# Performance work log

Measured on AMD Instinct MI355X. Metric: run time of the kernel, lower is better.

## Reference

```python
import jax, jax.numpy as jnp
import numpy as np

B, IN, OUT = 8192, 1024, 1024
GRID_SIZE, SPLINE_ORDER = 5, 3
GRID_LO, GRID_HI = -1.0, 1.0
LN_EPS = 1e-5


def make_grid():
    h = (GRID_HI - GRID_LO) / GRID_SIZE
    g = jnp.linspace(GRID_LO - h * SPLINE_ORDER, GRID_HI + h * SPLINE_ORDER,
                     GRID_SIZE + 2 * SPLINE_ORDER + 1, dtype=jnp.float32)
    return jnp.broadcast_to(g, (IN, g.shape[0]))  # [IN, 12]


def setup_inputs() -> dict:
    key = jax.random.key(0)
    k1, k2, k3 = jax.random.split(key, 3)
    # kaiming_uniform_ linear: bound = sqrt(3/fan_in)
    bw_bound = float(np.sqrt(3.0 / IN))
    sw_bound = float(np.sqrt(3.0 / (IN * 8)))
    return {
        "x": jax.random.normal(k1, (B, IN), dtype=jnp.float32),
        "base_weight": jax.random.uniform(k2, (OUT, IN), minval=-bw_bound, maxval=bw_bound, dtype=jnp.float32),
        "spline_weight": jax.random.uniform(k3, (OUT, IN, GRID_SIZE + SPLINE_ORDER), minval=-sw_bound, maxval=sw_bound, dtype=jnp.float32),
        "grid": make_grid(),
        "ln_gamma": jnp.ones((OUT,), dtype=jnp.float32),
        "ln_beta": jnp.zeros((OUT,), dtype=jnp.float32),
        "prelu_a": jnp.full((1,), 0.25, dtype=jnp.float32),
    }


def _bspline_bases(x, grid):
    # x: [B, IN]; grid: [IN, 12] -> bases: [B, IN, GRID_SIZE+SPLINE_ORDER]
    xu = x[:, :, None]                      # [B, IN, 1]
    g = grid[None, :, :]                    # [1, IN, 12]
    bases = ((xu >= g[..., :-1]) & (xu < g[..., 1:])).astype(x.dtype)
    for k in range(1, SPLINE_ORDER + 1):
        left = g[..., :-(k + 1)]
        right = g[..., k:-1]
        g_rshift = g[..., k + 1:]
        g_lshift = g[..., 1:-k]
        dr = right - left
        dd = g_rshift - g_lshift
        dr = jnp.where(dr == 0, jnp.ones_like(dr), dr)
        dd = jnp.where(dd == 0, jnp.ones_like(dd), dd)
        bases = (xu - left) / dr * bases[..., :-1] + (g_rshift - xu) / dd * bases[..., 1:]
    return bases


def reference(x, base_weight, spline_weight, grid, ln_gamma, ln_beta, prelu_a):
    base_out = jnp.dot(jax.nn.gelu(x, approximate=False), base_weight.T)  # [B, OUT]
    bases = _bspline_bases(x, grid)                                        # [B, IN, 8]
    spline_out = jnp.einsum('bik,oik->bo', bases, spline_weight)           # [B, OUT]
    y = base_out + spline_out
    mu = jnp.mean(y, axis=-1, keepdims=True)
    var = jnp.mean(jnp.square(y - mu), axis=-1, keepdims=True)
    yn = (y - mu) * jax.lax.rsqrt(var + LN_EPS) * ln_gamma + ln_beta
    return jnp.where(yn >= 0, yn, prelu_a * yn)
```

## Files before the change

### kernel.cpp

```cpp
#include <hip/hip_runtime.h>
#include <hip/hip_bf16.h>

typedef __attribute__((ext_vector_type(8))) short bf16x8;
typedef __attribute__((ext_vector_type(4))) float f32x4;

#define KTOT 9216
#define KHALF 4608
#define NB   8192
#define NIN  1024
#define NOUT 1024

__device__ __forceinline__ void load_lds16(const void* g, void* l) {
  __builtin_amdgcn_global_load_lds(
      (const __attribute__((address_space(1))) void*)g,
      (__attribute__((address_space(3))) void*)l, 16, 0, 0);
}

__global__ void prep(const float* __restrict__ x,
                     const float* __restrict__ grid,
                     __hip_bfloat16* __restrict__ A,
                     const float* __restrict__ bw,
                     const float* __restrict__ sw,
                     __hip_bfloat16* __restrict__ W) {
  if (blockIdx.x < 4096) {
    const int tid = blockIdx.x * blockDim.x + threadIdx.x;
    const int i  = tid & (NIN - 1);
    const int b0 = (tid >> 10) << 3;

    float g[12];
#pragma unroll
    for (int j = 0; j < 12; ++j) g[j] = grid[j];

    float invdr1[10], invdd1[10], invdr2[9], invdd2[9], invdr3[8], invdd3[8];
#pragma unroll
    for (int j = 0; j < 10; ++j) {
      invdr1[j] = __builtin_amdgcn_rcpf(g[j + 1] - g[j]);
      invdd1[j] = __builtin_amdgcn_rcpf(g[j + 2] - g[j + 1]);
    }
#pragma unroll
    for (int j = 0; j < 9; ++j) {
      invdr2[j] = __builtin_amdgcn_rcpf(g[j + 2] - g[j]);
      invdd2[j] = __builtin_amdgcn_rcpf(g[j + 3] - g[j + 1]);
    }
#pragma unroll
    for (int j = 0; j < 8; ++j) {
      invdr3[j] = __builtin_amdgcn_rcpf(g[j + 3] - g[j]);
      invdd3[j] = __builtin_amdgcn_rcpf(g[j + 4] - g[j + 1]);
    }

    for (int bb = 0; bb < 8; ++bb) {
      const int b = b0 + bb;
      const float xv = x[(size_t)b * NIN + i];
      const float ge = 0.5f * xv * (1.0f + erff(xv * 0.70710678118654752f));
      __hip_bfloat16* Arow = A + (size_t)b * KTOT;
      Arow[i] = __float2bfloat16(ge);

      float bas[11];
#pragma unroll
      for (int j = 0; j < 11; ++j)
        bas[j] = (xv >= g[j] && xv < g[j + 1]) ? 1.0f : 0.0f;
#pragma unroll
      for (int j = 0; j < 10; ++j)
        bas[j] = (xv - g[j]) * invdr1[j] * bas[j] + (g[j + 2] - xv) * invdd1[j] * bas[j + 1];
#pragma unroll
      for (int j = 0; j < 9; ++j)
        bas[j] = (xv - g[j]) * invdr2[j] * bas[j] + (g[j + 3] - xv) * invdd2[j] * bas[j + 1];
#pragma unroll
      for (int j = 0; j < 8; ++j)
        bas[j] = (xv - g[j]) * invdr3[j] * bas[j] + (g[j + 4] - xv) * invdd3[j] * bas[j + 1];

      union { __hip_bfloat16 h[8]; uint4 v; } u;
#pragma unroll
      for (int k = 0; k < 8; ++k) u.h[k] = __float2bfloat16(bas[k]);
      *reinterpret_cast<uint4*>(Arow + NIN + i * 8) = u.v;
    }
  } else {
    const int idx = (blockIdx.x - 4096) * blockDim.x + threadIdx.x;
    const int o  = idx / 1152;
    const int c8 = (idx - o * 1152) * 8;
    const float* src = (c8 < 1024) ? (bw + (size_t)o * 1024 + c8)
                                   : (sw + (size_t)o * 8192 + (c8 - 1024));
    float4 f0 = reinterpret_cast<const float4*>(src)[0];
    float4 f1 = reinterpret_cast<const float4*>(src)[1];
    union { __hip_bfloat16 h[8]; uint4 v; } u;
    u.h[0] = __float2bfloat16(f0.x); u.h[1] = __float2bfloat16(f0.y);
    u.h[2] = __float2bfloat16(f0.z); u.h[3] = __float2bfloat16(f0.w);
    u.h[4] = __float2bfloat16(f1.x); u.h[5] = __float2bfloat16(f1.y);
    u.h[6] = __float2bfloat16(f1.z); u.h[7] = __float2bfloat16(f1.w);
    *reinterpret_cast<uint4*>(W + (size_t)o * KTOT + c8) = u.v;
  }
}

__global__ __launch_bounds__(512, 2)
void gemm_8ph(const __hip_bfloat16* __restrict__ A,
              const __hip_bfloat16* __restrict__ Bw,
              float* __restrict__ P0,
              float* __restrict__ P1w) {
  extern __shared__ char smem[];

  const int tid  = threadIdx.x;
  const int lane = tid & 63;
  const int wave = tid >> 6;
  const int wr = wave >> 2;
  const int wc = wave & 3;

  const int orig = blockIdx.x;
  const int bid  = (orig & 7) * 32 + (orig >> 3);
  const int ks    = bid & 1;
  const int tileN = (bid >> 1) & 3;
  const int tileM = bid >> 3;
  const size_t brow = (size_t)tileM * 256;
  const size_t bcol = (size_t)tileN * 256;
  const int kbeg = ks * KHALF;

  const __hip_bfloat16* Ab = A  + brow * KTOT;
  const __hip_bfloat16* Bb = Bw + bcol * KTOT;
  float* C = ks ? P1w : P0;

  const int swsrc = ((tid & 7) ^ ((tid >> 3) & 7)) * 8;
  const __hip_bfloat16* srcA = Ab + (size_t)(tid >> 3) * KTOT + kbeg + swsrc;
  const __hip_bfloat16* srcB = Bb + (size_t)(tid >> 3) * KTOT + kbeg + swsrc;
  const int wdst = wave * 1024;

#define AHALF(buf, h) (smem + (buf) * 32768 + (h) * 16384)
#define BHALF(slot, h) (smem + 65536 + (slot) * 32768 + (h) * 16384)

  auto stageA = [&](int bufA, int h, int kt) {
    const __hip_bfloat16* g = srcA + (size_t)h * (128 * KTOT) + (size_t)kt * 64;
    char* d = AHALF(bufA, h) + wdst;
    load_lds16(g, d);
    load_lds16(g + (size_t)64 * KTOT, d + 8192);
  };
  auto stageB = [&](int slot, int h, int kt) {
    const __hip_bfloat16* g = srcB + (size_t)h * (128 * KTOT) + (size_t)kt * 64;
    char* d = BHALF(slot, h) + wdst;
    load_lds16(g, d);
    load_lds16(g + (size_t)64 * KTOT, d + 8192);
  };

  const int fr = lane & 15;
  const int hi = lane >> 4;
  const int sw = (fr & 7) << 4;
  const int ax0 = (hi * 16) ^ sw;
  const int ax1 = (64 + hi * 16) ^ sw;

  bf16x8 a[4][2], b[4][2];
  f32x4 acc[8][4] = {};

#define RD_A(CBA, MH) { \
    const char* Ah = AHALF(CBA, wr) + (MH) * 8192; \
    _Pragma("unroll") \
    for (int mi2 = 0; mi2 < 4; ++mi2) { \
      const char* p = Ah + (mi2 * 16 + fr) * 128; \
      a[mi2][0] = *(const bf16x8*)(p + ax0); \
      a[mi2][1] = *(const bf16x8*)(p + ax1); } }

#define RD_B(SB, NH) { \
    const char* Bh = BHALF(SB, wc >> 1) + ((wc & 1) * 64 + (NH) * 32) * 128; \
    _Pragma("unroll") \
    for (int ni2 = 0; ni2 < 2; ++ni2) { \
      const char* p = Bh + (ni2 * 16 + fr) * 128; \
      b[(NH) * 2 + ni2][0] = *(const bf16x8*)(p + ax0); \
      b[(NH) * 2 + ni2][1] = *(const bf16x8*)(p + ax1); } }

#define PH_SYNC() do { \
    asm volatile("" ::: "memory"); \
    __builtin_amdgcn_s_barrier(); \
    asm volatile("s_waitcnt lgkmcnt(0)" ::: "memory"); \
    __builtin_amdgcn_sched_barrier(0); } while (0)

#define QMFMA(MH, NH) do { \
    __builtin_amdgcn_s_setprio(1); \
    _Pragma("unroll") \
    for (int mi2 = 0; mi2 < 4; ++mi2) \
      _Pragma("unroll") \
      for (int ni2 = 0; ni2 < 2; ++ni2) \
        _Pragma("unroll") \
        for (int kk = 0; kk < 2; ++kk) \
          acc[(MH) * 4 + mi2][(NH) * 2 + ni2] = \
            __builtin_amdgcn_mfma_f32_16x16x32_bf16(a[mi2][kk], b[(NH) * 2 + ni2][kk], \
                                                    acc[(MH) * 4 + mi2][(NH) * 2 + ni2], 0, 0, 0); \
    __builtin_amdgcn_s_setprio(0); } while (0)

#define TILE(T, CBA, SB, SB2, STA, STB, VM2, VM4) do { \
     \
    RD_A(CBA, 0); RD_B(SB, 0); \
    if (STA) stageA((CBA) ^ 1, 0, (T) + 1); \
    PH_SYNC(); QMFMA(0, 0); \
     \
    RD_B(SB, 1); \
    if (STA) stageA((CBA) ^ 1, 1, (T) + 1); \
    asm volatile(VM2 ::: "memory"); \
    PH_SYNC(); QMFMA(0, 1); \
     \
    RD_A(CBA, 1); \
    if (STB) stageB(SB2, 0, (T) + 2); \
    PH_SYNC(); QMFMA(1, 1); \
     \
    if (STB) stageB(SB2, 1, (T) + 2); \
    asm volatile(VM4 ::: "memory"); \
    PH_SYNC(); QMFMA(1, 0); \
  } while (0)

  stageB(0, 0, 0); stageB(0, 1, 0);
  stageA(0, 0, 0); stageA(0, 1, 0);
  stageB(1, 0, 1); stageB(1, 1, 1);
  asm volatile("s_waitcnt vmcnt(6)" ::: "memory");
  __builtin_amdgcn_s_barrier();
  asm volatile("" ::: "memory");

  for (int it = 0; it < 11; ++it) {
    TILE(it * 6 + 0, 0, 0, 2, 1, 1, "s_waitcnt vmcnt(8)", "s_waitcnt vmcnt(6)");
    TILE(it * 6 + 1, 1, 1, 0, 1, 1, "s_waitcnt vmcnt(8)", "s_waitcnt vmcnt(6)");
    TILE(it * 6 + 2, 0, 2, 1, 1, 1, "s_waitcnt vmcnt(8)", "s_waitcnt vmcnt(6)");
    TILE(it * 6 + 3, 1, 0, 2, 1, 1, "s_waitcnt vmcnt(8)", "s_waitcnt vmcnt(6)");
    TILE(it * 6 + 4, 0, 1, 0, 1, 1, "s_waitcnt vmcnt(8)", "s_waitcnt vmcnt(6)");
    TILE(it * 6 + 5, 1, 2, 1, 1, 1, "s_waitcnt vmcnt(8)", "s_waitcnt vmcnt(6)");
  }
  TILE(66, 0, 0, 2, 1, 1, "s_waitcnt vmcnt(8)", "s_waitcnt vmcnt(6)");
  TILE(67, 1, 1, 0, 1, 1, "s_waitcnt vmcnt(8)", "s_waitcnt vmcnt(6)");
  TILE(68, 0, 2, 1, 1, 1, "s_waitcnt vmcnt(8)", "s_waitcnt vmcnt(6)");
  TILE(69, 1, 0, 2, 1, 1, "s_waitcnt vmcnt(8)", "s_waitcnt vmcnt(6)");
  TILE(70, 0, 1, 0, 1, 0, "s_waitcnt vmcnt(8)", "s_waitcnt vmcnt(2)");
  TILE(71, 1, 2, 1, 0, 0, "s_waitcnt vmcnt(0)", "s_nop 0");

#undef TILE
#undef QMFMA
#undef PH_SYNC
#undef RD_B
#undef RD_A
#undef BHALF
#undef AHALF

  const int crow0 = (lane >> 4) * 4;
#pragma unroll
  for (int mi = 0; mi < 8; ++mi)
#pragma unroll
    for (int ni = 0; ni < 4; ++ni) {
      const size_t r0 = brow + wr * 128 + mi * 16 + crow0;
      const size_t cc = bcol + wc * 64 + ni * 16 + fr;
      float* cp = C + r0 * NOUT + cc;
#pragma unroll
      for (int r = 0; r < 4; ++r) cp[(size_t)r * NOUT] = acc[mi][ni][r];
    }
}

__global__ void reduce_ln_prelu(const float* __restrict__ P0,
                                float* __restrict__ y,
                                const float* __restrict__ gamma,
                                const float* __restrict__ beta,
                                const float* __restrict__ pa) {
  const int row = blockIdx.x;
  const int t = threadIdx.x;
  const float* p0r = P0 + (size_t)row * NOUT;
  float* yr = y + (size_t)row * NOUT;

  float4 aa = reinterpret_cast<const float4*>(p0r)[t];
  float4 v = reinterpret_cast<const float4*>(yr)[t];
  v.x += aa.x; v.y += aa.y; v.z += aa.z; v.w += aa.w;

  float s  = v.x + v.y + v.z + v.w;
  float sq = v.x * v.x + v.y * v.y + v.z * v.z + v.w * v.w;
#pragma unroll
  for (int off = 32; off > 0; off >>= 1) {
    s  += __shfl_down(s, off);
    sq += __shfl_down(sq, off);
  }
  __shared__ float red[8];
  const int wv = t >> 6, lane = t & 63;
  if (lane == 0) { red[wv] = s; red[4 + wv] = sq; }
  __syncthreads();
  if (t == 0) {
    const float S = red[0] + red[1] + red[2] + red[3];
    const float Q = red[4] + red[5] + red[6] + red[7];
    const float mu = S * (1.0f / NOUT);
    const float var = Q * (1.0f / NOUT) - mu * mu;
    red[0] = mu;
    red[1] = rsqrtf(var + 1e-5f);
  }
  __syncthreads();
  const float mu = red[0], rs = red[1];
  const float aP = pa[0];
  const float4 g4 = reinterpret_cast<const float4*>(gamma)[t];
  const float4 b4 = reinterpret_cast<const float4*>(beta)[t];
  float o0 = (v.x - mu) * rs * g4.x + b4.x;
  float o1 = (v.y - mu) * rs * g4.y + b4.y;
  float o2 = (v.z - mu) * rs * g4.z + b4.z;
  float o3 = (v.w - mu) * rs * g4.w + b4.w;
  v.x = o0 >= 0.0f ? o0 : aP * o0;
  v.y = o1 >= 0.0f ? o1 : aP * o1;
  v.z = o2 >= 0.0f ? o2 : aP * o2;
  v.w = o3 >= 0.0f ? o3 : aP * o3;
  reinterpret_cast<float4*>(yr)[t] = v;
}

extern "C" void kernel_launch(void* const* d_in, const int* in_sizes, int n_in,
                              void* d_out, int out_size, void* d_ws, size_t ws_size,
                              hipStream_t stream) {
  const float* x     = (const float*)d_in[0];
  const float* bw    = (const float*)d_in[1];
  const float* sw    = (const float*)d_in[2];
  const float* grid  = (const float*)d_in[3];
  const float* gamma = (const float*)d_in[4];
  const float* beta  = (const float*)d_in[5];
  const float* pa    = (const float*)d_in[6];
  float* out = (float*)d_out;

  __hip_bfloat16* Abuf = (__hip_bfloat16*)d_ws;
  __hip_bfloat16* Wbuf = Abuf + (size_t)NB * KTOT;
  float* P0 = (float*)(Wbuf + (size_t)NOUT * KTOT);

  hipFuncSetAttribute(reinterpret_cast<const void*>(gemm_8ph),
                      hipFuncAttributeMaxDynamicSharedMemorySize, 163840);

  prep<<<4096 + 4608, 256, 0, stream>>>(x, grid, Abuf, bw, sw, Wbuf);
  gemm_8ph<<<(NB / 256) * (NOUT / 256) * 2, 512, 163840, stream>>>(Abuf, Wbuf, P0, out);
  reduce_ln_prelu<<<NB, 256, 0, stream>>>(P0, out, gamma, beta, pa);
}
```

Measured before the change: 198.7 us.

## Restructure GEMM pipeline to two phases per tile with triple-buffered A

Reworks the main GEMM k-loop from four barrier phases per K-tile to two. A is now triple-buffered (prefetched two tiles ahead) and B double-buffered (one tile ahead), where before A was double- and B triple-buffered. Each phase issues larger batches of LDS reads and MFMAs between barriers, cutting synchronisation overhead. In exchange there is less fine-grained interleaving of loads with compute, and B loads have less time to land, which could expose memory latency.

```diff
diff --git a/kernel.cpp b/kernel.cpp
--- a/kernel.cpp
+++ b/kernel.cpp
@@ -92,10 +92,10 @@
 }
 
 __global__ __launch_bounds__(512, 2)
-void gemm_8ph(const __hip_bfloat16* __restrict__ A,
-              const __hip_bfloat16* __restrict__ Bw,
-              float* __restrict__ P0,
-              float* __restrict__ P1w) {
+void gemm_2b(const __hip_bfloat16* __restrict__ A,
+             const __hip_bfloat16* __restrict__ Bw,
+             float* __restrict__ P0,
+             float* __restrict__ P1w) {
   extern __shared__ char smem[];
 
   const int tid  = threadIdx.x;
@@ -122,18 +122,18 @@
   const __hip_bfloat16* srcB = Bb + (size_t)(tid >> 3) * KTOT + kbeg + swsrc;
   const int wdst = wave * 1024;
 
-#define AHALF(buf, h) (smem + (buf) * 32768 + (h) * 16384)
-#define BHALF(slot, h) (smem + 65536 + (slot) * 32768 + (h) * 16384)
-
-  auto stageA = [&](int bufA, int h, int kt) {
+#define AB_(buf)  (smem + (buf) * 32768)
+#define BB_(slot) (smem + 98304 + (slot) * 32768)
+
+  auto stageA = [&](int buf, int h, int kt) {
     const __hip_bfloat16* g = srcA + (size_t)h * (128 * KTOT) + (size_t)kt * 64;
-    char* d = AHALF(bufA, h) + wdst;
+    char* d = AB_(buf) + h * 16384 + wdst;
     load_lds16(g, d);
     load_lds16(g + (size_t)64 * KTOT, d + 8192);
   };
   auto stageB = [&](int slot, int h, int kt) {
     const __hip_bfloat16* g = srcB + (size_t)h * (128 * KTOT) + (size_t)kt * 64;
-    char* d = BHALF(slot, h) + wdst;
+    char* d = BB_(slot) + h * 16384 + wdst;
     load_lds16(g, d);
     load_lds16(g + (size_t)64 * KTOT, d + 8192);
   };
@@ -147,16 +147,16 @@
   bf16x8 a[4][2], b[4][2];
   f32x4 acc[8][4] = {};
 
-#define RD_A(CBA, MH) { \
-    const char* Ah = AHALF(CBA, wr) + (MH) * 8192; \
+#define RD_A(BUF, MH) { \
+    const char* Ah = AB_(BUF) + wr * 16384 + (MH) * 8192; \
     _Pragma("unroll") \
     for (int mi2 = 0; mi2 < 4; ++mi2) { \
       const char* p = Ah + (mi2 * 16 + fr) * 128; \
       a[mi2][0] = *(const bf16x8*)(p + ax0); \
       a[mi2][1] = *(const bf16x8*)(p + ax1); } }
 
-#define RD_B(SB, NH) { \
-    const char* Bh = BHALF(SB, wc >> 1) + ((wc & 1) * 64 + (NH) * 32) * 128; \
+#define RD_B(SLOT, NH) { \
+    const char* Bh = BB_(SLOT) + (wc >> 1) * 16384 + ((wc & 1) * 64 + (NH) * 32) * 128; \
     _Pragma("unroll") \
     for (int ni2 = 0; ni2 < 2; ++ni2) { \
       const char* p = Bh + (ni2 * 16 + fr) * 128; \
@@ -182,55 +182,50 @@
                                                     acc[(MH) * 4 + mi2][(NH) * 2 + ni2], 0, 0, 0); \
     __builtin_amdgcn_s_setprio(0); } while (0)
 
-#define TILE(T, CBA, SB, SB2, STA, STB, VM2, VM4) do { \
+#define TILE(T, ABUF, A2, BSL, STB, STA, VMB) do { \
      \
-    RD_A(CBA, 0); RD_B(SB, 0); \
-    if (STA) stageA((CBA) ^ 1, 0, (T) + 1); \
-    PH_SYNC(); QMFMA(0, 0); \
+    RD_A(ABUF, 0); RD_B(BSL, 0); RD_B(BSL, 1); \
+    if (STB) { stageB((BSL) ^ 1, 0, (T) + 1); stageB((BSL) ^ 1, 1, (T) + 1); } \
+    PH_SYNC(); \
+    QMFMA(0, 0); QMFMA(0, 1); \
      \
-    RD_B(SB, 1); \
-    if (STA) stageA((CBA) ^ 1, 1, (T) + 1); \
-    asm volatile(VM2 ::: "memory"); \
-    PH_SYNC(); QMFMA(0, 1); \
-     \
-    RD_A(CBA, 1); \
-    if (STB) stageB(SB2, 0, (T) + 2); \
-    PH_SYNC(); QMFMA(1, 1); \
-     \
-    if (STB) stageB(SB2, 1, (T) + 2); \
-    asm volatile(VM4 ::: "memory"); \
-    PH_SYNC(); QMFMA(1, 0); \
+    RD_A(ABUF, 1); \
+    if (STA) { stageA(A2, 0, (T) + 2); stageA(A2, 1, (T) + 2); } \
+    asm volatile(VMB ::: "memory"); \
+    PH_SYNC(); \
+    QMFMA(1, 1); QMFMA(1, 0); \
   } while (0)
 
+  stageA(0, 0, 0); stageA(0, 1, 0);
   stageB(0, 0, 0); stageB(0, 1, 0);
-  stageA(0, 0, 0); stageA(0, 1, 0);
-  stageB(1, 0, 1); stageB(1, 1, 1);
-  asm volatile("s_waitcnt vmcnt(6)" ::: "memory");
+  stageA(1, 0, 1); stageA(1, 1, 1);
+  asm volatile("s_waitcnt vmcnt(4)" ::: "memory");
   __builtin_amdgcn_s_barrier();
   asm volatile("" ::: "memory");
 
   for (int it = 0; it < 11; ++it) {
-    TILE(it * 6 + 0, 0, 0, 2, 1, 1, "s_waitcnt vmcnt(8)", "s_waitcnt vmcnt(6)");
-    TILE(it * 6 + 1, 1, 1, 0, 1, 1, "s_waitcnt vmcnt(8)", "s_waitcnt vmcnt(6)");
-    TILE(it * 6 + 2, 0, 2, 1, 1, 1, "s_waitcnt vmcnt(8)", "s_waitcnt vmcnt(6)");
-    TILE(it * 6 + 3, 1, 0, 2, 1, 1, "s_waitcnt vmcnt(8)", "s_waitcnt vmcnt(6)");
-    TILE(it * 6 + 4, 0, 1, 0, 1, 1, "s_waitcnt vmcnt(8)", "s_waitcnt vmcnt(6)");
-    TILE(it * 6 + 5, 1, 2, 1, 1, 1, "s_waitcnt vmcnt(8)", "s_waitcnt vmcnt(6)");
+    const int t0 = it * 6;
+    TILE(t0 + 0, 0, 2, 0, 1, 1, "s_waitcnt vmcnt(4)");
+    TILE(t0 + 1, 1, 0, 1, 1, 1, "s_waitcnt vmcnt(4)");
+    TILE(t0 + 2, 2, 1, 0, 1, 1, "s_waitcnt vmcnt(4)");
+    TILE(t0 + 3, 0, 2, 1, 1, 1, "s_waitcnt vmcnt(4)");
+    TILE(t0 + 4, 1, 0, 0, 1, 1, "s_waitcnt vmcnt(4)");
+    TILE(t0 + 5, 2, 1, 1, 1, 1, "s_waitcnt vmcnt(4)");
   }
-  TILE(66, 0, 0, 2, 1, 1, "s_waitcnt vmcnt(8)", "s_waitcnt vmcnt(6)");
-  TILE(67, 1, 1, 0, 1, 1, "s_waitcnt vmcnt(8)", "s_waitcnt vmcnt(6)");
-  TILE(68, 0, 2, 1, 1, 1, "s_waitcnt vmcnt(8)", "s_waitcnt vmcnt(6)");
-  TILE(69, 1, 0, 2, 1, 1, "s_waitcnt vmcnt(8)", "s_waitcnt vmcnt(6)");
-  TILE(70, 0, 1, 0, 1, 0, "s_waitcnt vmcnt(8)", "s_waitcnt vmcnt(2)");
-  TILE(71, 1, 2, 1, 0, 0, "s_waitcnt vmcnt(0)", "s_nop 0");
+  TILE(66, 0, 2, 0, 1, 1, "s_waitcnt vmcnt(4)");
+  TILE(67, 1, 0, 1, 1, 1, "s_waitcnt vmcnt(4)");
+  TILE(68, 2, 1, 0, 1, 1, "s_waitcnt vmcnt(4)");
+  TILE(69, 0, 2, 1, 1, 1, "s_waitcnt vmcnt(4)");
+  TILE(70, 1, 0, 0, 1, 0, "s_waitcnt vmcnt(0)");
+  TILE(71, 2, 1, 1, 0, 0, "s_nop 0");
 
 #undef TILE
 #undef QMFMA
 #undef PH_SYNC
 #undef RD_B
 #undef RD_A
-#undef BHALF
-#undef AHALF
+#undef BB_
+#undef AB_
 
   const int crow0 = (lane >> 4) * 4;
 #pragma unroll
@@ -310,10 +305,10 @@
   __hip_bfloat16* Wbuf = Abuf + (size_t)NB * KTOT;
   float* P0 = (float*)(Wbuf + (size_t)NOUT * KTOT);
 
-  hipFuncSetAttribute(reinterpret_cast<const void*>(gemm_8ph),
+  hipFuncSetAttribute(reinterpret_cast<const void*>(gemm_2b),
                       hipFuncAttributeMaxDynamicSharedMemorySize, 163840);
 
   prep<<<4096 + 4608, 256, 0, stream>>>(x, grid, Abuf, bw, sw, Wbuf);
-  gemm_8ph<<<(NB / 256) * (NOUT / 256) * 2, 512, 163840, stream>>>(Abuf, Wbuf, P0, out);
+  gemm_2b<<<(NB / 256) * (NOUT / 256) * 2, 512, 163840, stream>>>(Abuf, Wbuf, P0, out);
   reduce_ln_prelu<<<NB, 256, 0, stream>>>(P0, out, gamma, beta, pa);
 }
```

After: 197.4 us. No clear change (-0.6%).
